# Performance work log

Hardware: AMD Instinct MI355X
Metric: run time of the kernel (lower is better)

The kernel has to match this reference:

```python
import jax, jax.numpy as jnp
import numpy as np

B, N_IN, O, IN_L, OUT_L = 256, 1152, 10, 8, 16
ITERS = 3
EPS = 1e-7

def squash(s, eps):
    # norm over the capsule-length axis (-2), keepdim, as in the torch code
    dot = jnp.sum(s * s, axis=-2, keepdims=True)
    return (dot / (1.0 + dot) / jnp.sqrt(dot + eps)) * s

def setup_inputs() -> dict:
    key = jax.random.key(0)
    k1, k2, k3 = jax.random.split(key, 3)
    x = jax.random.normal(k1, (B, N_IN, IN_L, 1), dtype=jnp.float32)
    weight = 0.05 * jax.random.normal(k2, (1, N_IN, O, IN_L, OUT_L), dtype=jnp.float32)
    bias = 0.05 * jax.random.normal(k3, (1, 1, O, OUT_L, 1), dtype=jnp.float32)
    return {"x": x, "weight": weight, "bias": bias}

def reference(x, weight, bias):
    # u_hat[b,n,o,k] = sum_i W[0,n,o,i,k] * x[b,n,i,0]  -> (B, N, O, K, 1)
    u_hat = jnp.einsum('noik,bni->bnok', weight[0], x[..., 0])[..., None]
    u_det = jax.lax.stop_gradient(u_hat)
    b_ij = jnp.zeros((x.shape[0], N_IN, O, 1, 1), dtype=x.dtype)
    v = None
    for r in range(ITERS):
        c = jax.nn.softmax(b_ij, axis=2)          # routing coefficients over out caps
        u = u_hat if r == ITERS - 1 else u_det    # detached except last iter
        s = jnp.sum(c * u, axis=1, keepdims=True) + bias  # (B,1,O,K,1)
        v = squash(s, EPS)
        if r != ITERS - 1:
            # agreement: sum over capsule-length axis 3 -> (B,N,O,1,1)
            b_ij = b_ij + jnp.sum(u_det * v, axis=3, keepdims=True)
    return v
```

## Files before the change

kernel.cpp:

```cpp
#include <hip/hip_runtime.h>
#include <hip/hip_bf16.h>

#define BB   256
#define NIN  1152
#define OO   10
#define IL   8
#define OL   16
#define ROW  (OO*OL)
#define EPSQ 1e-7f
#define NT   8
#define BT   32

typedef unsigned short ushx8 __attribute__((ext_vector_type(8)));
typedef unsigned short ushx4 __attribute__((ext_vector_type(4)));

__device__ __forceinline__ float bf2f(unsigned short h) {
    unsigned u = ((unsigned)h) << 16;
    return __builtin_bit_cast(float, u);
}

__global__ __launch_bounds__(160) void caps_build(
    const float* __restrict__ x, const float* __restrict__ w,
    unsigned short* __restrict__ u)
{
    __shared__ float4 wl4[NT][321];
    __shared__ float4 xl4[BT * 16];
    const int t  = threadIdx.x;
    const int n0 = blockIdx.x * NT;
    const int b0 = blockIdx.y * BT;

    const float4* wg = reinterpret_cast<const float4*>(w) + (size_t)n0 * 320;
    for (int j = t; j < NT * 320; j += 160) {
        const int row = j / 320;
        const int lin = j - row * 320;
        const int o   = lin >> 5;
        const int rem = lin & 31;
        const int i   = rem >> 2;
        const int kh  = rem & 3;
        const int ip  = i ^ (o & 1);
        wl4[row][(o << 5) | (ip << 2) | kh] = wg[j];
    }
    const float4* xg = reinterpret_cast<const float4*>(x);
    for (int j = t; j < BT * 16; j += 160) {
        const int bl = j >> 4;
        const int r  = j & 15;
        xl4[j] = xg[((size_t)(b0 + bl) * NIN + n0) * 2 + r];
    }
    __syncthreads();

    const int nl = t / 20;
    const int s  = t - nl * 20;
    const int o  = s >> 1;
    const int k8 = s & 1;
    const int p  = o & 1;
    const float4* wbase = &wl4[nl][(o << 5) | (k8 << 1)];
    const float4* xbase = &xl4[nl * 2];
    unsigned short* ub = u + ((size_t)b0 * NIN + n0 + nl) * ROW + o * OL + k8 * 8;
    const size_t ustride = (size_t)NIN * ROW;

    for (int bl = 0; bl < BT; bl += 2) {
        const float4 xa0 = xbase[bl * 16];
        const float4 xa1 = xbase[bl * 16 + 1];
        const float4 xb0 = xbase[bl * 16 + 16];
        const float4 xb1 = xbase[bl * 16 + 17];
        const float xv0[IL] = {xa0.x, xa0.y, xa0.z, xa0.w, xa1.x, xa1.y, xa1.z, xa1.w};
        const float xv1[IL] = {xb0.x, xb0.y, xb0.z, xb0.w, xb1.x, xb1.y, xb1.z, xb1.w};

        float a0[8] = {0,0,0,0,0,0,0,0};
        float a1[8] = {0,0,0,0,0,0,0,0};
        #pragma unroll
        for (int i = 0; i < IL; ++i) {
            const float4 wlo = wbase[(i ^ p) << 2];
            const float4 whi = wbase[((i ^ p) << 2) | 1];
            const float wv[8] = {wlo.x, wlo.y, wlo.z, wlo.w, whi.x, whi.y, whi.z, whi.w};
            #pragma unroll
            for (int j = 0; j < 8; ++j) {
                a0[j] = fmaf(wv[j], xv0[i], a0[j]);
                a1[j] = fmaf(wv[j], xv1[i], a1[j]);
            }
        }
        union { ushx8 v; __hip_bfloat162 h[4]; } p0, p1;
        #pragma unroll
        for (int j = 0; j < 4; ++j) {
            p0.h[j] = __float22bfloat162_rn(make_float2(a0[2*j], a0[2*j+1]));
            p1.h[j] = __float22bfloat162_rn(make_float2(a1[2*j], a1[2*j+1]));
        }
        *reinterpret_cast<ushx8*>(ub + (size_t)bl * ustride)       = p0.v;
        *reinterpret_cast<ushx8*>(ub + (size_t)(bl + 1) * ustride) = p1.v;
    }
}

__global__ __launch_bounds__(768) void caps_route3(
    const unsigned short* __restrict__ u, const float* __restrict__ bias,
    float* __restrict__ outv)
{
    __shared__ float lds[12][ROW];
    __shared__ float vbuf[ROW];
    const int t  = threadIdx.x;
    const int q  = t & 3;
    const int g  = t >> 2;
    const int wv = t >> 6;
    const int b  = blockIdx.x;
    const unsigned short* ub = u + (size_t)b * NIN * ROW + (q << 2);

    float bsv = 0.f;
    if (t < ROW) bsv = bias[t];
    float vprev = 0.f;

    float4 sp[OO];

    #pragma unroll
    for (int iter = 0; iter < 3; ++iter) {
        #pragma unroll
        for (int o = 0; o < OO; ++o) sp[o] = make_float4(0.f, 0.f, 0.f, 0.f);

        if (iter == 0) {
            for (int m = 0; m < 6; ++m) {
                const unsigned short* un = ub + (size_t)(g + m * 192) * ROW;
                #pragma unroll
                for (int o = 0; o < OO; ++o) {
                    const ushx4 raw = *reinterpret_cast<const ushx4*>(un + o * OL);
                    sp[o].x += bf2f(raw[0]);
                    sp[o].y += bf2f(raw[1]);
                    sp[o].z += bf2f(raw[2]);
                    sp[o].w += bf2f(raw[3]);
                }
            }
        } else {
            float4 vs[OO];
            #pragma unroll
            for (int o = 0; o < OO; ++o)
                vs[o] = *reinterpret_cast<const float4*>(&vbuf[o * OL + (q << 2)]);

            for (int m = 0; m < 6; ++m) {
                const unsigned short* un = ub + (size_t)(g + m * 192) * ROW;
                ushx4 raw[OO];
                #pragma unroll
                for (int o = 0; o < OO; ++o)
                    raw[o] = *reinterpret_cast<const ushx4*>(un + o * OL);

                float bij[OO];
                #pragma unroll
                for (int o = 0; o < OO; ++o) {
                    float d = bf2f(raw[o][0]) * vs[o].x;
                    d = fmaf(bf2f(raw[o][1]), vs[o].y, d);
                    d = fmaf(bf2f(raw[o][2]), vs[o].z, d);
                    d = fmaf(bf2f(raw[o][3]), vs[o].w, d);
                    d += __shfl_xor(d, 1, 4);
                    d += __shfl_xor(d, 2, 4);
                    bij[o] = d;
                }
                float mx = bij[0];
                #pragma unroll
                for (int o = 1; o < OO; ++o) mx = fmaxf(mx, bij[o]);
                float e[OO], se = 0.f;
                #pragma unroll
                for (int o = 0; o < OO; ++o) { e[o] = __expf(bij[o] - mx); se += e[o]; }
                const float r = 1.f / se;
                #pragma unroll
                for (int o = 0; o < OO; ++o) {
                    const float c = e[o] * r;
                    sp[o].x = fmaf(c, bf2f(raw[o][0]), sp[o].x);
                    sp[o].y = fmaf(c, bf2f(raw[o][1]), sp[o].y);
                    sp[o].z = fmaf(c, bf2f(raw[o][2]), sp[o].z);
                    sp[o].w = fmaf(c, bf2f(raw[o][3]), sp[o].w);
                }
            }
        }

        #pragma unroll
        for (int o = 0; o < OO; ++o) {
            #pragma unroll
            for (int msk = 4; msk <= 32; msk <<= 1) {
                sp[o].x += __shfl_xor(sp[o].x, msk);
                sp[o].y += __shfl_xor(sp[o].y, msk);
                sp[o].z += __shfl_xor(sp[o].z, msk);
                sp[o].w += __shfl_xor(sp[o].w, msk);
            }
        }
        if ((t & 63) < 4) {
            #pragma unroll
            for (int o = 0; o < OO; ++o) {
                lds[wv][o * OL + q * 4 + 0] = sp[o].x;
                lds[wv][o * OL + q * 4 + 1] = sp[o].y;
                lds[wv][o * OL + q * 4 + 2] = sp[o].z;
                lds[wv][o * OL + q * 4 + 3] = sp[o].w;
            }
        }
        __syncthreads();

        if (t < ROW) {
            float ssum = 0.f;
            #pragma unroll
            for (int wvi = 0; wvi < 12; ++wvi) ssum += lds[wvi][t];
            const float sv = (iter == 0 ? 0.1f : 1.0f) * ssum + bsv;

            float d = sv * sv;
            d += __shfl_xor(d, 1, 16);
            d += __shfl_xor(d, 2, 16);
            d += __shfl_xor(d, 4, 16);
            d += __shfl_xor(d, 8, 16);
            const float f = d / ((1.f + d) * sqrtf(d + EPSQ));
            const float v = f * sv;

            if (iter == 0) { vbuf[t] = v; vprev = v; }
            else if (iter == 1) { vbuf[t] = v + vprev; }
            else { outv[(size_t)b * ROW + t] = v; }
        }
        __syncthreads();
    }
}

extern "C" void kernel_launch(void* const* d_in, const int* in_sizes, int n_in,
                              void* d_out, int out_size, void* d_ws, size_t ws_size,
                              hipStream_t stream) {
    const float* x    = (const float*)d_in[0];
    const float* w    = (const float*)d_in[1];
    const float* bias = (const float*)d_in[2];
    float* out = (float*)d_out;

    unsigned short* u = (unsigned short*)d_ws;

    caps_build<<<dim3(NIN / NT, BB / BT), 160, 0, stream>>>(x, w, u);
    caps_route3<<<BB, 768, 0, stream>>>(u, bias, out);
}
```

Before: 87.58 us.

## Widen routing loads to 16-byte chunks and process four batches per build pass

The routing kernel now has each lane of a 4-lane group read 8 contiguous bf16 values (half an output capsule) instead of 4 values per capsule. Loads become 16 bytes wide and each group needs one fewer shuffle for the agreement dot product, with the softmax over the two halves exchanged by a single xor-2 shuffle. The build kernel computes four batch rows per loop step instead of two, so each weight load from LDS is reused more often. The cost is more registers (40 floats of accumulator per thread in routing, 32 in build), which could lower occupancy.

New measurement: 85.56 us. 2.3% less time.

```diff
diff --git a/kernel.cpp b/kernel.cpp
--- a/kernel.cpp
+++ b/kernel.cpp
@@ -58,35 +58,42 @@
     unsigned short* ub = u + ((size_t)b0 * NIN + n0 + nl) * ROW + o * OL + k8 * 8;
     const size_t ustride = (size_t)NIN * ROW;
 
-    for (int bl = 0; bl < BT; bl += 2) {
-        const float4 xa0 = xbase[bl * 16];
-        const float4 xa1 = xbase[bl * 16 + 1];
-        const float4 xb0 = xbase[bl * 16 + 16];
-        const float4 xb1 = xbase[bl * 16 + 17];
-        const float xv0[IL] = {xa0.x, xa0.y, xa0.z, xa0.w, xa1.x, xa1.y, xa1.z, xa1.w};
-        const float xv1[IL] = {xb0.x, xb0.y, xb0.z, xb0.w, xb1.x, xb1.y, xb1.z, xb1.w};
-
-        float a0[8] = {0,0,0,0,0,0,0,0};
-        float a1[8] = {0,0,0,0,0,0,0,0};
+    for (int bl = 0; bl < BT; bl += 4) {
+        float xv[4][IL];
+        #pragma unroll
+        for (int bb = 0; bb < 4; ++bb) {
+            const float4 x0 = xbase[(bl + bb) * 16];
+            const float4 x1 = xbase[(bl + bb) * 16 + 1];
+            xv[bb][0] = x0.x; xv[bb][1] = x0.y; xv[bb][2] = x0.z; xv[bb][3] = x0.w;
+            xv[bb][4] = x1.x; xv[bb][5] = x1.y; xv[bb][6] = x1.z; xv[bb][7] = x1.w;
+        }
+
+        float acc[4][8];
+        #pragma unroll
+        for (int bb = 0; bb < 4; ++bb)
+            #pragma unroll
+            for (int j = 0; j < 8; ++j) acc[bb][j] = 0.f;
+
         #pragma unroll
         for (int i = 0; i < IL; ++i) {
             const float4 wlo = wbase[(i ^ p) << 2];
             const float4 whi = wbase[((i ^ p) << 2) | 1];
             const float wv[8] = {wlo.x, wlo.y, wlo.z, wlo.w, whi.x, whi.y, whi.z, whi.w};
             #pragma unroll
-            for (int j = 0; j < 8; ++j) {
-                a0[j] = fmaf(wv[j], xv0[i], a0[j]);
-                a1[j] = fmaf(wv[j], xv1[i], a1[j]);
-            }
-        }
-        union { ushx8 v; __hip_bfloat162 h[4]; } p0, p1;
-        #pragma unroll
-        for (int j = 0; j < 4; ++j) {
-            p0.h[j] = __float22bfloat162_rn(make_float2(a0[2*j], a0[2*j+1]));
-            p1.h[j] = __float22bfloat162_rn(make_float2(a1[2*j], a1[2*j+1]));
-        }
-        *reinterpret_cast<ushx8*>(ub + (size_t)bl * ustride)       = p0.v;
-        *reinterpret_cast<ushx8*>(ub + (size_t)(bl + 1) * ustride) = p1.v;
+            for (int bb = 0; bb < 4; ++bb)
+                #pragma unroll
+                for (int j = 0; j < 8; ++j)
+                    acc[bb][j] = fmaf(wv[j], xv[bb][i], acc[bb][j]);
+        }
+
+        #pragma unroll
+        for (int bb = 0; bb < 4; ++bb) {
+            union { ushx8 v; __hip_bfloat162 h[4]; } pk;
+            #pragma unroll
+            for (int j = 0; j < 4; ++j)
+                pk.h[j] = __float22bfloat162_rn(make_float2(acc[bb][2*j], acc[bb][2*j+1]));
+            *reinterpret_cast<ushx8*>(ub + (size_t)(bl + bb) * ustride) = pk.v;
+        }
     }
 }
 
@@ -101,91 +108,94 @@
     const int g  = t >> 2;
     const int wv = t >> 6;
     const int b  = blockIdx.x;
-    const unsigned short* ub = u + (size_t)b * NIN * ROW + (q << 2);
+    const unsigned short* ub = u + (size_t)b * NIN * ROW;
 
     float bsv = 0.f;
     if (t < ROW) bsv = bias[t];
     float vprev = 0.f;
 
-    float4 sp[OO];
-
     #pragma unroll
     for (int iter = 0; iter < 3; ++iter) {
-        #pragma unroll
-        for (int o = 0; o < OO; ++o) sp[o] = make_float4(0.f, 0.f, 0.f, 0.f);
+        float sp[5][8];
+        #pragma unroll
+        for (int j = 0; j < 5; ++j)
+            #pragma unroll
+            for (int e = 0; e < 8; ++e) sp[j][e] = 0.f;
 
         if (iter == 0) {
             for (int m = 0; m < 6; ++m) {
                 const unsigned short* un = ub + (size_t)(g + m * 192) * ROW;
                 #pragma unroll
-                for (int o = 0; o < OO; ++o) {
-                    const ushx4 raw = *reinterpret_cast<const ushx4*>(un + o * OL);
-                    sp[o].x += bf2f(raw[0]);
-                    sp[o].y += bf2f(raw[1]);
-                    sp[o].z += bf2f(raw[2]);
-                    sp[o].w += bf2f(raw[3]);
+                for (int j = 0; j < 5; ++j) {
+                    const ushx8 raw = *reinterpret_cast<const ushx8*>(un + (q + 4 * j) * 8);
+                    #pragma unroll
+                    for (int e = 0; e < 8; ++e) sp[j][e] += bf2f(raw[e]);
                 }
             }
         } else {
-            float4 vs[OO];
-            #pragma unroll
-            for (int o = 0; o < OO; ++o)
-                vs[o] = *reinterpret_cast<const float4*>(&vbuf[o * OL + (q << 2)]);
+            float vs[5][8];
+            #pragma unroll
+            for (int j = 0; j < 5; ++j) {
+                #pragma unroll
+                for (int e = 0; e < 8; ++e) vs[j][e] = vbuf[(q + 4 * j) * 8 + e];
+            }
 
             for (int m = 0; m < 6; ++m) {
                 const unsigned short* un = ub + (size_t)(g + m * 192) * ROW;
-                ushx4 raw[OO];
-                #pragma unroll
-                for (int o = 0; o < OO; ++o)
-                    raw[o] = *reinterpret_cast<const ushx4*>(un + o * OL);
-
-                float bij[OO];
-                #pragma unroll
-                for (int o = 0; o < OO; ++o) {
-                    float d = bf2f(raw[o][0]) * vs[o].x;
-                    d = fmaf(bf2f(raw[o][1]), vs[o].y, d);
-                    d = fmaf(bf2f(raw[o][2]), vs[o].z, d);
-                    d = fmaf(bf2f(raw[o][3]), vs[o].w, d);
-                    d += __shfl_xor(d, 1, 4);
-                    d += __shfl_xor(d, 2, 4);
-                    bij[o] = d;
-                }
-                float mx = bij[0];
-                #pragma unroll
-                for (int o = 1; o < OO; ++o) mx = fmaxf(mx, bij[o]);
-                float e[OO], se = 0.f;
-                #pragma unroll
-                for (int o = 0; o < OO; ++o) { e[o] = __expf(bij[o] - mx); se += e[o]; }
+                float uf[5][8];
+                #pragma unroll
+                for (int j = 0; j < 5; ++j) {
+                    const ushx8 raw = *reinterpret_cast<const ushx8*>(un + (q + 4 * j) * 8);
+                    #pragma unroll
+                    for (int e = 0; e < 8; ++e) uf[j][e] = bf2f(raw[e]);
+                }
+
+                float d[5], dd[5];
+                #pragma unroll
+                for (int j = 0; j < 5; ++j) {
+                    float acc = uf[j][0] * vs[j][0];
+                    #pragma unroll
+                    for (int e = 1; e < 8; ++e) acc = fmaf(uf[j][e], vs[j][e], acc);
+                    acc += __shfl_xor(acc, 1, 4);
+                    d[j] = acc;
+                }
+                #pragma unroll
+                for (int j = 0; j < 5; ++j) dd[j] = __shfl_xor(d[j], 2, 4);
+
+                float mx = fmaxf(d[0], dd[0]);
+                #pragma unroll
+                for (int j = 1; j < 5; ++j) mx = fmaxf(mx, fmaxf(d[j], dd[j]));
+                float se = 0.f, e_[5];
+                #pragma unroll
+                for (int j = 0; j < 5; ++j) {
+                    e_[j] = __expf(d[j] - mx);
+                    se += e_[j] + __expf(dd[j] - mx);
+                }
                 const float r = 1.f / se;
                 #pragma unroll
-                for (int o = 0; o < OO; ++o) {
-                    const float c = e[o] * r;
-                    sp[o].x = fmaf(c, bf2f(raw[o][0]), sp[o].x);
-                    sp[o].y = fmaf(c, bf2f(raw[o][1]), sp[o].y);
-                    sp[o].z = fmaf(c, bf2f(raw[o][2]), sp[o].z);
-                    sp[o].w = fmaf(c, bf2f(raw[o][3]), sp[o].w);
-                }
-            }
-        }
-
-        #pragma unroll
-        for (int o = 0; o < OO; ++o) {
-            #pragma unroll
-            for (int msk = 4; msk <= 32; msk <<= 1) {
-                sp[o].x += __shfl_xor(sp[o].x, msk);
-                sp[o].y += __shfl_xor(sp[o].y, msk);
-                sp[o].z += __shfl_xor(sp[o].z, msk);
-                sp[o].w += __shfl_xor(sp[o].w, msk);
-            }
-        }
+                for (int j = 0; j < 5; ++j) {
+                    const float c = e_[j] * r;
+                    #pragma unroll
+                    for (int e = 0; e < 8; ++e)
+                        sp[j][e] = fmaf(c, uf[j][e], sp[j][e]);
+                }
+            }
+        }
+
+        #pragma unroll
+        for (int j = 0; j < 5; ++j)
+            #pragma unroll
+            for (int e = 0; e < 8; ++e) {
+                #pragma unroll
+                for (int msk = 4; msk <= 32; msk <<= 1)
+                    sp[j][e] += __shfl_xor(sp[j][e], msk);
+            }
         if ((t & 63) < 4) {
             #pragma unroll
-            for (int o = 0; o < OO; ++o) {
-                lds[wv][o * OL + q * 4 + 0] = sp[o].x;
-                lds[wv][o * OL + q * 4 + 1] = sp[o].y;
-                lds[wv][o * OL + q * 4 + 2] = sp[o].z;
-                lds[wv][o * OL + q * 4 + 3] = sp[o].w;
-            }
+            for (int j = 0; j < 5; ++j)
+                #pragma unroll
+                for (int e = 0; e < 8; ++e)
+                    lds[wv][(q + 4 * j) * 8 + e] = sp[j][e];
         }
         __syncthreads();
 
@@ -195,12 +205,12 @@
             for (int wvi = 0; wvi < 12; ++wvi) ssum += lds[wvi][t];
             const float sv = (iter == 0 ? 0.1f : 1.0f) * ssum + bsv;
 
-            float d = sv * sv;
-            d += __shfl_xor(d, 1, 16);
-            d += __shfl_xor(d, 2, 16);
-            d += __shfl_xor(d, 4, 16);
-            d += __shfl_xor(d, 8, 16);
-            const float f = d / ((1.f + d) * sqrtf(d + EPSQ));
+            float dq = sv * sv;
+            dq += __shfl_xor(dq, 1, 16);
+            dq += __shfl_xor(dq, 2, 16);
+            dq += __shfl_xor(dq, 4, 16);
+            dq += __shfl_xor(dq, 8, 16);
+            const float f = dq / ((1.f + dq) * sqrtf(dq + EPSQ));
             const float v = f * sv;
 
             if (iter == 0) { vbuf[t] = v; vprev = v; }
```
